# Performance work log

Hardware: AMD Instinct MI355X
Metric: run time of the kernel (lower is better)

Reference implementation:

```python
import jax, jax.numpy as jnp
import numpy as np

# Qwen3-VL-MoE text experts (training path): token permute -> grouped GEMM
# (gate_up) -> SwiGLU -> grouped GEMM (down) -> token unpermute + prob combine.
# Routing is generated perfectly balanced (each expert receives exactly M/E
# expanded tokens) so the grouped GEMM over the sorted token buffer is exactly
# a batched matmul over E contiguous groups -- same math as npu_grouped_matmul.

E, H, D, T, K = 32, 2048, 768, 4096, 8  # experts, hidden, moe_intermediate, tokens, top_k
M = T * K                                # expanded rows


def setup_inputs() -> dict:
    key = jax.random.key(0)
    k1, k2, k3, k4, k5 = jax.random.split(key, 5)
    hidden_states = jax.random.normal(k1, (T, H), dtype=jnp.float32)
    routing_weights = jax.nn.softmax(jax.random.normal(k2, (T, E), dtype=jnp.float32), axis=-1)
    # balanced expert assignment: each expert id appears exactly M // E times
    flat = jnp.tile(jnp.arange(E, dtype=jnp.int32), M // E)
    router_indices = jax.random.permutation(k3, flat).reshape(T, K)
    gate_up_proj = jax.random.normal(k4, (E, H, 2 * D), dtype=jnp.float32) * 0.02
    down_proj = jax.random.normal(k5, (E, D, H), dtype=jnp.float32) * 0.02
    return {
        "hidden_states": hidden_states,
        "routing_weights": routing_weights,
        "router_indices": router_indices,
        "gate_up_proj": gate_up_proj,
        "down_proj": down_proj,
    }


def reference(hidden_states, routing_weights, router_indices, gate_up_proj, down_proj):
    n_tok, hid = hidden_states.shape
    n_exp = gate_up_proj.shape[0]
    top_k = router_indices.shape[1]
    n_rows = n_tok * top_k
    grp = n_rows // n_exp  # balanced group size

    # --- npu_moe_token_permute: sort expanded (token, slot) rows by expert id
    flat_experts = router_indices.reshape(-1)            # (M,)
    order = jnp.argsort(flat_experts)                    # stable sort by expert
    permuted = hidden_states[order // top_k]             # (M, H)

    # --- grouped GEMM #1 (gate_up): balanced groups -> batched matmul
    xg = permuted.reshape(n_exp, grp, hid)               # (E, g, H)
    gate_up = jnp.einsum('egh,ehd->egd', xg, gate_up_proj)  # (E, g, 2D)

    # --- npu_swiglu(dim=-1): silu(first half) * second half
    gate, up = jnp.split(gate_up, 2, axis=-1)
    act = jax.nn.silu(gate) * up                         # (E, g, D)

    # --- grouped GEMM #2 (down)
    out = jnp.einsum('egd,edh->egh', act, down_proj).reshape(n_rows, hid)

    # --- npu_moe_token_unpermute: invert permutation, combine with probs
    inv = jnp.argsort(order)
    expanded = out[inv].reshape(n_tok, top_k, hid)       # (T, K, H)
    probs = jnp.take_along_axis(routing_weights, router_indices, axis=1)  # (T, K)
    return jnp.einsum('tkh,tk->th', expanded, probs)     # (T, H)
```

## Files before the change

### kernel.cpp

```cpp
#include <hip/hip_runtime.h>
#include <hip/hip_bf16.h>
#include <cstdint>


#define E_   32
#define H_   2048
#define D_   768
#define T_   4096
#define K_   8
#define M_   (T_ * K_)
#define G_   (M_ / E_)
#define GU2  (2 * D_)

typedef unsigned short u16;
typedef short bf16x8 __attribute__((ext_vector_type(8)));
typedef float f32x4 __attribute__((ext_vector_type(4)));
typedef unsigned short u16x2 __attribute__((ext_vector_type(2)));
typedef unsigned short u16x8 __attribute__((ext_vector_type(8)));

__device__ __forceinline__ u16 f2bf(float f) {
  unsigned u = __float_as_uint(f);
  u += 0x7FFFu + ((u >> 16) & 1u);
  return (u16)(u >> 16);
}
__device__ __forceinline__ float bf2f(u16 v) {
  return __uint_as_float(((unsigned)v) << 16);
}

#define GLOAD16(g, l) __builtin_amdgcn_global_load_lds(                        \
    (const __attribute__((address_space(1))) void*)(g),                        \
    (__attribute__((address_space(3))) void*)(l), 16, 0, 0)

#define VM8()   asm volatile("s_waitcnt vmcnt(8)" ::: "memory")
#define VM4()   asm volatile("s_waitcnt vmcnt(4)" ::: "memory")
#define VM0()   asm volatile("s_waitcnt vmcnt(0)" ::: "memory")
#define LGKM0() asm volatile("s_waitcnt lgkmcnt(0)" ::: "memory")
#define SCHB()  __builtin_amdgcn_sched_barrier(0)
#define BAR()   __builtin_amdgcn_s_barrier()

__global__ __launch_bounds__(256) void cvt_hidden(const float* __restrict__ in,
                                                  u16* __restrict__ out) {
  const int i = blockIdx.x * 256 + threadIdx.x;
  const float4 v = ((const float4*)in)[i];
  u16x2 a; a.x = f2bf(v.x); a.y = f2bf(v.y);
  u16x2 b; b.x = f2bf(v.z); b.y = f2bf(v.w);
  *(u16x2*)&out[(size_t)i * 4]     = a;
  *(u16x2*)&out[(size_t)i * 4 + 2] = b;
}

__global__ __launch_bounds__(256) void transpose_cvt(const float* __restrict__ in,
                                                     u16* __restrict__ out,
                                                     int R, int C, int mode) {
  __shared__ u16 tl[64 * 72];
  const int b = blockIdx.z;
  const int c0 = blockIdx.x * 64, r0 = blockIdx.y * 64;
  const int tid = threadIdx.x;
  const float* ip = in + ((size_t)b * R + r0) * C + c0;
  const int rr4 = tid >> 4;
  const int cc4 = (tid & 15) * 4;
#pragma unroll
  for (int p = 0; p < 4; ++p) {
    const int r = p * 16 + rr4;
    const float4 v = *(const float4*)&ip[(size_t)r * C + cc4];
    tl[(cc4 + 0) * 72 + r] = f2bf(v.x);
    tl[(cc4 + 1) * 72 + r] = f2bf(v.y);
    tl[(cc4 + 2) * 72 + r] = f2bf(v.z);
    tl[(cc4 + 3) * 72 + r] = f2bf(v.w);
  }
  __syncthreads();
  const int rs = (tid & 7) * 8;
#pragma unroll
  for (int q = 0; q < 2; ++q) {
    const int c = q * 32 + (tid >> 3);
    const int gc = c0 + c;
    int rr;
    if (mode == 1) {
      const int j = (gc < D_) ? gc : (gc - D_);
      rr = (j >> 4) * 32 + ((gc < D_) ? 0 : 16) + (j & 15);
    } else {
      rr = gc;
    }
    const u16x8 v = *(const u16x8*)&tl[c * 72 + rs];
    *(u16x8*)&out[((size_t)b * C + rr) * R + r0 + rs] = v;
  }
}

__global__ __launch_bounds__(256) void build_perm(const int* __restrict__ ridx,
                                                  int* __restrict__ perm_src) {
  const int e = blockIdx.x;
  const int lane = threadIdx.x & 63, wid = threadIdx.x >> 6;
  __shared__ int wcnt[4];
  __shared__ int running;
  if (threadIdx.x == 0) running = 0;
  __syncthreads();
  for (int base = 0; base < M_; base += 256) {
    const int i = base + threadIdx.x;
    const bool match = (ridx[i] == e);
    const unsigned long long mask = __ballot(match);
    if (lane == 0) wcnt[wid] = __popcll(mask);
    __syncthreads();
    int wpre = 0;
    for (int w0 = 0; w0 < wid; ++w0) wpre += wcnt[w0];
    const int rank = __popcll(mask & ((1ull << lane) - 1ull));
    if (match) perm_src[e * G_ + running + wpre + rank] = i;
    __syncthreads();
    if (threadIdx.x == 0) running += wcnt[0] + wcnt[1] + wcnt[2] + wcnt[3];
    __syncthreads();
  }
}

__global__ __launch_bounds__(256) void gather_probs(const int* __restrict__ ridx,
                                                    const float* __restrict__ rw,
                                                    float* __restrict__ probs) {
  const int i = blockIdx.x * 256 + threadIdx.x;
  const int t = i >> 3;
  probs[i] = rw[t * E_ + ridx[i]];
}

__global__ __launch_bounds__(512, 2) void gemm1_swiglu(
    const u16* __restrict__ hid, const u16* __restrict__ gup,
    const int* __restrict__ perm, u16* __restrict__ act) {
  __shared__ u16 As[4][8192];
  __shared__ u16 Bs[4][8192];
  const int NT = H_ / 32;

  const int nwg = 6 * 4 * E_;
  const int wid = (blockIdx.x % 8) * (nwg / 8) + blockIdx.x / 8;
  const int e = wid / 24;
  const int mb = (wid / 6) % 4;
  const int nb = wid % 6;

  const int tid = threadIdx.x;
  const int lane = tid & 63, w = tid >> 6;
  const int wr = w >> 2, wc = w & 3;

  const int srow = tid >> 2, schunk = tid & 3;
  const u16* pA[2]; const u16* pB[2];
#pragma unroll
  for (int q = 0; q < 2; ++q) {
    const int r = q * 128 + srow;
    const int cg = (schunk ^ ((r >> 1) & 3)) * 8;
    const int token = perm[e * G_ + mb * 256 + r] >> 3;
    pA[q] = hid + (size_t)token * H_ + cg;
    pB[q] = gup + ((size_t)e * GU2 + nb * 256 + r) * H_ + cg;
  }

  int aoff[8], boff[4];
  {
    const int l15 = lane & 15, hk = lane >> 4;
#pragma unroll
    for (int m = 0; m < 8; ++m) {
      const int rA = wr * 128 + m * 16 + l15;
      aoff[m] = rA * 32 + ((hk ^ ((rA >> 1) & 3)) * 8);
    }
#pragma unroll
    for (int n = 0; n < 4; ++n) {
      const int rB = wc * 64 + n * 16 + l15;
      boff[n] = rB * 32 + ((hk ^ ((rB >> 1) & 3)) * 8);
    }
  }

  f32x4 acc[8][4];
#pragma unroll
  for (int m = 0; m < 8; ++m)
#pragma unroll
    for (int n = 0; n < 4; ++n) acc[m][n] = (f32x4){0.f, 0.f, 0.f, 0.f};

  GLOAD16(pA[0], &As[0][tid * 8]);      GLOAD16(pA[1], &As[0][4096 + tid * 8]);
  GLOAD16(pB[0], &Bs[0][tid * 8]);      GLOAD16(pB[1], &Bs[0][4096 + tid * 8]);
  GLOAD16(pA[0] + 32, &As[1][tid * 8]); GLOAD16(pA[1] + 32, &As[1][4096 + tid * 8]);
  GLOAD16(pB[0] + 32, &Bs[1][tid * 8]); GLOAD16(pB[1] + 32, &Bs[1][4096 + tid * 8]);
  GLOAD16(pA[0] + 64, &As[2][tid * 8]); GLOAD16(pA[1] + 64, &As[2][4096 + tid * 8]);
  GLOAD16(pB[0] + 64, &Bs[2][tid * 8]); GLOAD16(pB[1] + 64, &Bs[2][4096 + tid * 8]);
  VM8(); BAR(); SCHB();

#pragma unroll 4
  for (int t = 0; t < NT; ++t) {
    const int slot = t & 3, ts = (t + 3) & 3;
    const bool st = (t + 3) < NT;
    const u16* Ab = As[slot]; const u16* Bb = Bs[slot];
    bf16x8 av[4], bv[4];
#pragma unroll
    for (int n = 0; n < 4; ++n) bv[n] = *(const bf16x8*)&Bb[boff[n]];
#pragma unroll
    for (int m = 0; m < 4; ++m) av[m] = *(const bf16x8*)&Ab[aoff[m]];
    if (st) {
      GLOAD16(pA[0] + (t + 3) * 32, &As[ts][tid * 8]);
      GLOAD16(pA[1] + (t + 3) * 32, &As[ts][4096 + tid * 8]);
    }
    SCHB(); BAR(); LGKM0(); SCHB();
    __builtin_amdgcn_s_setprio(1);
#pragma unroll
    for (int m = 0; m < 4; ++m)
#pragma unroll
      for (int n = 0; n < 4; ++n)
        acc[m][n] = __builtin_amdgcn_mfma_f32_16x16x32_bf16(av[m], bv[n],
                                                            acc[m][n], 0, 0, 0);
    __builtin_amdgcn_s_setprio(0);
    SCHB(); BAR();
#pragma unroll
    for (int m = 0; m < 4; ++m) av[m] = *(const bf16x8*)&Ab[aoff[m + 4]];
    if (st) {
      GLOAD16(pB[0] + (t + 3) * 32, &Bs[ts][tid * 8]);
      GLOAD16(pB[1] + (t + 3) * 32, &Bs[ts][4096 + tid * 8]);
    }
    SCHB(); BAR(); LGKM0(); SCHB();
    __builtin_amdgcn_s_setprio(1);
#pragma unroll
    for (int m = 0; m < 4; ++m)
#pragma unroll
      for (int n = 0; n < 4; ++n)
        acc[m + 4][n] = __builtin_amdgcn_mfma_f32_16x16x32_bf16(av[m], bv[n],
                                                                acc[m + 4][n], 0, 0, 0);
    __builtin_amdgcn_s_setprio(0);
    SCHB();
    if (t + 3 < NT)      { VM8(); }
    else if (t + 2 < NT) { VM4(); }
    else                 { VM0(); }
    BAR();
  }

  const int lrow = (lane >> 4) * 4, lcol = lane & 15;
#pragma unroll
  for (int m = 0; m < 8; ++m)
#pragma unroll
    for (int p = 0; p < 2; ++p)
#pragma unroll
      for (int r = 0; r < 4; ++r) {
        const float g = acc[m][2 * p][r];
        const float u = acc[m][2 * p + 1][r];
        const float a_ = g / (1.f + __expf(-g)) * u;
        const int row = mb * 256 + wr * 128 + m * 16 + lrow + r;
        const int dcol = (nb * 8 + wc * 2 + p) * 16 + lcol;
        act[((size_t)e * G_ + row) * D_ + dcol] = f2bf(a_);
      }
}

__global__ __launch_bounds__(512, 2) void gemm2_scatter(
    const u16* __restrict__ act, const u16* __restrict__ dwn,
    const int* __restrict__ perm, u16* __restrict__ expo) {
  __shared__ u16 As[4][8192];
  __shared__ u16 Bs[4][8192];
  const int NT = D_ / 32;

  const int nwg = 8 * 4 * E_;
  const int wid = (blockIdx.x % 8) * (nwg / 8) + blockIdx.x / 8;
  const int e = wid / 32;
  const int mb = (wid / 8) % 4;
  const int nb = wid % 8;

  const int tid = threadIdx.x;
  const int lane = tid & 63, w = tid >> 6;
  const int wr = w >> 2, wc = w & 3;

  const int srow = tid >> 2, schunk = tid & 3;
  const u16* pA[2]; const u16* pB[2];
#pragma unroll
  for (int q = 0; q < 2; ++q) {
    const int r = q * 128 + srow;
    const int cg = (schunk ^ ((r >> 1) & 3)) * 8;
    pA[q] = act + ((size_t)e * G_ + mb * 256 + r) * D_ + cg;
    pB[q] = dwn + ((size_t)e * H_ + nb * 256 + r) * D_ + cg;
  }

  int aoff[8], boff[4];
  {
    const int l15 = lane & 15, hk = lane >> 4;
#pragma unroll
    for (int m = 0; m < 8; ++m) {
      const int rA = wr * 128 + m * 16 + l15;
      aoff[m] = rA * 32 + ((hk ^ ((rA >> 1) & 3)) * 8);
    }
#pragma unroll
    for (int n = 0; n < 4; ++n) {
      const int rB = wc * 64 + n * 16 + l15;
      boff[n] = rB * 32 + ((hk ^ ((rB >> 1) & 3)) * 8);
    }
  }

  f32x4 acc[8][4];
#pragma unroll
  for (int m = 0; m < 8; ++m)
#pragma unroll
    for (int n = 0; n < 4; ++n) acc[m][n] = (f32x4){0.f, 0.f, 0.f, 0.f};

  GLOAD16(pA[0], &As[0][tid * 8]);      GLOAD16(pA[1], &As[0][4096 + tid * 8]);
  GLOAD16(pB[0], &Bs[0][tid * 8]);      GLOAD16(pB[1], &Bs[0][4096 + tid * 8]);
  GLOAD16(pA[0] + 32, &As[1][tid * 8]); GLOAD16(pA[1] + 32, &As[1][4096 + tid * 8]);
  GLOAD16(pB[0] + 32, &Bs[1][tid * 8]); GLOAD16(pB[1] + 32, &Bs[1][4096 + tid * 8]);
  GLOAD16(pA[0] + 64, &As[2][tid * 8]); GLOAD16(pA[1] + 64, &As[2][4096 + tid * 8]);
  GLOAD16(pB[0] + 64, &Bs[2][tid * 8]); GLOAD16(pB[1] + 64, &Bs[2][4096 + tid * 8]);
  VM8(); BAR(); SCHB();

#pragma unroll 4
  for (int t = 0; t < NT; ++t) {
    const int slot = t & 3, ts = (t + 3) & 3;
    const bool st = (t + 3) < NT;
    const u16* Ab = As[slot]; const u16* Bb = Bs[slot];
    bf16x8 av[4], bv[4];
#pragma unroll
    for (int n = 0; n < 4; ++n) bv[n] = *(const bf16x8*)&Bb[boff[n]];
#pragma unroll
    for (int m = 0; m < 4; ++m) av[m] = *(const bf16x8*)&Ab[aoff[m]];
    if (st) {
      GLOAD16(pA[0] + (t + 3) * 32, &As[ts][tid * 8]);
      GLOAD16(pA[1] + (t + 3) * 32, &As[ts][4096 + tid * 8]);
    }
    SCHB(); BAR(); LGKM0(); SCHB();
    __builtin_amdgcn_s_setprio(1);
#pragma unroll
    for (int m = 0; m < 4; ++m)
#pragma unroll
      for (int n = 0; n < 4; ++n)
        acc[m][n] = __builtin_amdgcn_mfma_f32_16x16x32_bf16(av[m], bv[n],
                                                            acc[m][n], 0, 0, 0);
    __builtin_amdgcn_s_setprio(0);
    SCHB(); BAR();
#pragma unroll
    for (int m = 0; m < 4; ++m) av[m] = *(const bf16x8*)&Ab[aoff[m + 4]];
    if (st) {
      GLOAD16(pB[0] + (t + 3) * 32, &Bs[ts][tid * 8]);
      GLOAD16(pB[1] + (t + 3) * 32, &Bs[ts][4096 + tid * 8]);
    }
    SCHB(); BAR(); LGKM0(); SCHB();
    __builtin_amdgcn_s_setprio(1);
#pragma unroll
    for (int m = 0; m < 4; ++m)
#pragma unroll
      for (int n = 0; n < 4; ++n)
        acc[m + 4][n] = __builtin_amdgcn_mfma_f32_16x16x32_bf16(av[m], bv[n],
                                                                acc[m + 4][n], 0, 0, 0);
    __builtin_amdgcn_s_setprio(0);
    SCHB();
    if (t + 3 < NT)      { VM8(); }
    else if (t + 2 < NT) { VM4(); }
    else                 { VM0(); }
    BAR();
  }

  const int lrow = (lane >> 4) * 4, lcol = lane & 15;
#pragma unroll
  for (int m = 0; m < 8; ++m)
#pragma unroll
    for (int r = 0; r < 4; ++r) {
      const int dst = e * G_ + mb * 256 + wr * 128 + m * 16 + lrow + r;
      const int src = perm[dst];
      u16* orow = expo + (size_t)src * H_ + nb * 256 + wc * 64;
#pragma unroll
      for (int n = 0; n < 4; ++n)
        orow[n * 16 + lcol] = f2bf(acc[m][n][r]);
    }
}

__global__ __launch_bounds__(256) void combine(const u16* __restrict__ expo,
                                               const float* __restrict__ probs,
                                               float* __restrict__ out) {
  const int t = blockIdx.x;
  const int h0 = threadIdx.x * 8;
  float r[8] = {0.f, 0.f, 0.f, 0.f, 0.f, 0.f, 0.f, 0.f};
#pragma unroll
  for (int k = 0; k < K_; ++k) {
    const float p = probs[t * K_ + k];
    const u16x8 v = *(const u16x8*)&expo[((size_t)(t * K_ + k)) * H_ + h0];
#pragma unroll
    for (int j = 0; j < 8; ++j) r[j] += p * bf2f(v[j]);
  }
  float4 o0 = {r[0], r[1], r[2], r[3]};
  float4 o1 = {r[4], r[5], r[6], r[7]};
  *(float4*)&out[(size_t)t * H_ + h0]     = o0;
  *(float4*)&out[(size_t)t * H_ + h0 + 4] = o1;
}

extern "C" void kernel_launch(void* const* d_in, const int* in_sizes, int n_in,
                              void* d_out, int out_size, void* d_ws, size_t ws_size,
                              hipStream_t stream) {
  const float* hidden = (const float*)d_in[0];
  const float* rw     = (const float*)d_in[1];
  const int*   ridx   = (const int*)d_in[2];
  const float* gup_f  = (const float*)d_in[3];
  const float* dwn_f  = (const float*)d_in[4];
  float* out = (float*)d_out;

  char* ws = (char*)d_ws;
  size_t off = 0;
  auto alloc = [&](size_t bytes) -> void* {
    void* p = ws + off;
    off += (bytes + 255) & ~(size_t)255;
    return p;
  };
  u16*   hid_bf = (u16*)alloc((size_t)T_ * H_ * 2);
  u16*   gup_t  = (u16*)alloc((size_t)E_ * GU2 * H_ * 2);
  u16*   dwn_t  = (u16*)alloc((size_t)E_ * H_ * D_ * 2);
  u16*   act    = (u16*)alloc((size_t)M_ * D_ * 2);
  u16*   expo   = (u16*)alloc((size_t)M_ * H_ * 2);
  int*   perm   = (int*)alloc((size_t)M_ * 4);
  float* probs  = (float*)alloc((size_t)M_ * 4);
  if (off > ws_size) return;

  cvt_hidden<<<(T_ * H_ / 4) / 256, 256, 0, stream>>>(hidden, hid_bf);
  transpose_cvt<<<dim3(GU2 / 64, H_ / 64, E_), 256, 0, stream>>>(gup_f, gup_t, H_, GU2, 1);
  transpose_cvt<<<dim3(H_ / 64, D_ / 64, E_), 256, 0, stream>>>(dwn_f, dwn_t, D_, H_, 0);
  build_perm<<<E_, 256, 0, stream>>>(ridx, perm);
  gather_probs<<<M_ / 256, 256, 0, stream>>>(ridx, rw, probs);
  gemm1_swiglu<<<6 * 4 * E_, 512, 0, stream>>>(hid_bf, gup_t, perm, act);
  gemm2_scatter<<<8 * 4 * E_, 512, 0, stream>>>(act, dwn_t, perm, expo);
  combine<<<T_, 256, 0, stream>>>(expo, probs, out);
}
```

Measured before the change: 618.6 us.

## Switch grouped GEMMs to 32x32 MFMA and parallelize permutation build

Result: faster. 564.2 us (-8.8%).

```diff
diff --git a/kernel.cpp b/kernel.cpp
--- a/kernel.cpp
+++ b/kernel.cpp
@@ -14,7 +14,7 @@
 
 typedef unsigned short u16;
 typedef short bf16x8 __attribute__((ext_vector_type(8)));
-typedef float f32x4 __attribute__((ext_vector_type(4)));
+typedef float f32x16 __attribute__((ext_vector_type(16)));
 typedef unsigned short u16x2 __attribute__((ext_vector_type(2)));
 typedef unsigned short u16x8 __attribute__((ext_vector_type(8)));
 
@@ -76,7 +76,7 @@
     int rr;
     if (mode == 1) {
       const int j = (gc < D_) ? gc : (gc - D_);
-      rr = (j >> 4) * 32 + ((gc < D_) ? 0 : 16) + (j & 15);
+      rr = (j >> 5) * 64 + ((gc < D_) ? 0 : 32) + (j & 31);
     } else {
       rr = gc;
     }
@@ -85,36 +85,21 @@
   }
 }
 
-__global__ __launch_bounds__(256) void build_perm(const int* __restrict__ ridx,
-                                                  int* __restrict__ perm_src) {
-  const int e = blockIdx.x;
-  const int lane = threadIdx.x & 63, wid = threadIdx.x >> 6;
-  __shared__ int wcnt[4];
-  __shared__ int running;
-  if (threadIdx.x == 0) running = 0;
+__global__ __launch_bounds__(256) void build_perm_fast(const int* __restrict__ ridx,
+                                                       int* __restrict__ perm,
+                                                       int* __restrict__ gcnt) {
+  __shared__ int lc[E_];
+  __shared__ int lb[E_];
+  const int tid = threadIdx.x;
+  if (tid < E_) lc[tid] = 0;
   __syncthreads();
-  for (int base = 0; base < M_; base += 256) {
-    const int i = base + threadIdx.x;
-    const bool match = (ridx[i] == e);
-    const unsigned long long mask = __ballot(match);
-    if (lane == 0) wcnt[wid] = __popcll(mask);
-    __syncthreads();
-    int wpre = 0;
-    for (int w0 = 0; w0 < wid; ++w0) wpre += wcnt[w0];
-    const int rank = __popcll(mask & ((1ull << lane) - 1ull));
-    if (match) perm_src[e * G_ + running + wpre + rank] = i;
-    __syncthreads();
-    if (threadIdx.x == 0) running += wcnt[0] + wcnt[1] + wcnt[2] + wcnt[3];
-    __syncthreads();
-  }
-}
-
-__global__ __launch_bounds__(256) void gather_probs(const int* __restrict__ ridx,
-                                                    const float* __restrict__ rw,
-                                                    float* __restrict__ probs) {
-  const int i = blockIdx.x * 256 + threadIdx.x;
-  const int t = i >> 3;
-  probs[i] = rw[t * E_ + ridx[i]];
+  const int i = blockIdx.x * 256 + tid;
+  const int e = ridx[i];
+  const int p = atomicAdd(&lc[e], 1);
+  __syncthreads();
+  if (tid < E_) lb[tid] = atomicAdd(&gcnt[tid], lc[tid]);
+  __syncthreads();
+  perm[e * G_ + lb[e] + p] = i;
 }
 
 __global__ __launch_bounds__(512, 2) void gemm1_swiglu(
@@ -145,26 +130,30 @@
     pB[q] = gup + ((size_t)e * GU2 + nb * 256 + r) * H_ + cg;
   }
 
-  int aoff[8], boff[4];
-  {
-    const int l15 = lane & 15, hk = lane >> 4;
-#pragma unroll
-    for (int m = 0; m < 8; ++m) {
-      const int rA = wr * 128 + m * 16 + l15;
-      aoff[m] = rA * 32 + ((hk ^ ((rA >> 1) & 3)) * 8);
-    }
-#pragma unroll
-    for (int n = 0; n < 4; ++n) {
-      const int rB = wc * 64 + n * 16 + l15;
-      boff[n] = rB * 32 + ((hk ^ ((rB >> 1) & 3)) * 8);
-    }
-  }
-
-  f32x4 acc[8][4];
-#pragma unroll
-  for (int m = 0; m < 8; ++m)
-#pragma unroll
-    for (int n = 0; n < 4; ++n) acc[m][n] = (f32x4){0.f, 0.f, 0.f, 0.f};
+  const int l31 = lane & 31, hi = lane >> 5;
+  int aoff[4][2], boff[2][2];
+#pragma unroll
+  for (int m = 0; m < 4; ++m) {
+    const int rA = wr * 128 + m * 32 + l31;
+#pragma unroll
+    for (int ks = 0; ks < 2; ++ks)
+      aoff[m][ks] = rA * 32 + (((ks * 2 + hi) ^ ((rA >> 1) & 3)) * 8);
+  }
+#pragma unroll
+  for (int n = 0; n < 2; ++n) {
+    const int rB = wc * 64 + n * 32 + l31;
+#pragma unroll
+    for (int ks = 0; ks < 2; ++ks)
+      boff[n][ks] = rB * 32 + (((ks * 2 + hi) ^ ((rB >> 1) & 3)) * 8);
+  }
+
+  f32x16 acc[4][2];
+#pragma unroll
+  for (int m = 0; m < 4; ++m)
+#pragma unroll
+    for (int n = 0; n < 2; ++n)
+#pragma unroll
+      for (int r = 0; r < 16; ++r) acc[m][n][r] = 0.f;
 
   GLOAD16(pA[0], &As[0][tid * 8]);      GLOAD16(pA[1], &As[0][4096 + tid * 8]);
   GLOAD16(pB[0], &Bs[0][tid * 8]);      GLOAD16(pB[1], &Bs[0][4096 + tid * 8]);
@@ -179,11 +168,11 @@
     const int slot = t & 3, ts = (t + 3) & 3;
     const bool st = (t + 3) < NT;
     const u16* Ab = As[slot]; const u16* Bb = Bs[slot];
-    bf16x8 av[4], bv[4];
-#pragma unroll
-    for (int n = 0; n < 4; ++n) bv[n] = *(const bf16x8*)&Bb[boff[n]];
-#pragma unroll
-    for (int m = 0; m < 4; ++m) av[m] = *(const bf16x8*)&Ab[aoff[m]];
+    bf16x8 av[4], bv[2];
+#pragma unroll
+    for (int n = 0; n < 2; ++n) bv[n] = *(const bf16x8*)&Bb[boff[n][0]];
+#pragma unroll
+    for (int m = 0; m < 4; ++m) av[m] = *(const bf16x8*)&Ab[aoff[m][0]];
     if (st) {
       GLOAD16(pA[0] + (t + 3) * 32, &As[ts][tid * 8]);
       GLOAD16(pA[1] + (t + 3) * 32, &As[ts][4096 + tid * 8]);
@@ -193,13 +182,15 @@
 #pragma unroll
     for (int m = 0; m < 4; ++m)
 #pragma unroll
-      for (int n = 0; n < 4; ++n)
-        acc[m][n] = __builtin_amdgcn_mfma_f32_16x16x32_bf16(av[m], bv[n],
+      for (int n = 0; n < 2; ++n)
+        acc[m][n] = __builtin_amdgcn_mfma_f32_32x32x16_bf16(av[m], bv[n],
                                                             acc[m][n], 0, 0, 0);
     __builtin_amdgcn_s_setprio(0);
     SCHB(); BAR();
 #pragma unroll
-    for (int m = 0; m < 4; ++m) av[m] = *(const bf16x8*)&Ab[aoff[m + 4]];
+    for (int n = 0; n < 2; ++n) bv[n] = *(const bf16x8*)&Bb[boff[n][1]];
+#pragma unroll
+    for (int m = 0; m < 4; ++m) av[m] = *(const bf16x8*)&Ab[aoff[m][1]];
     if (st) {
       GLOAD16(pB[0] + (t + 3) * 32, &Bs[ts][tid * 8]);
       GLOAD16(pB[1] + (t + 3) * 32, &Bs[ts][4096 + tid * 8]);
@@ -209,9 +200,9 @@
 #pragma unroll
     for (int m = 0; m < 4; ++m)
 #pragma unroll
-      for (int n = 0; n < 4; ++n)
-        acc[m + 4][n] = __builtin_amdgcn_mfma_f32_16x16x32_bf16(av[m], bv[n],
-                                                                acc[m + 4][n], 0, 0, 0);
+      for (int n = 0; n < 2; ++n)
+        acc[m][n] = __builtin_amdgcn_mfma_f32_32x32x16_bf16(av[m], bv[n],
+                                                            acc[m][n], 0, 0, 0);
     __builtin_amdgcn_s_setprio(0);
     SCHB();
     if (t + 3 < NT)      { VM8(); }
@@ -220,20 +211,17 @@
     BAR();
   }
 
-  const int lrow = (lane >> 4) * 4, lcol = lane & 15;
-#pragma unroll
-  for (int m = 0; m < 8; ++m)
-#pragma unroll
-    for (int p = 0; p < 2; ++p)
-#pragma unroll
-      for (int r = 0; r < 4; ++r) {
-        const float g = acc[m][2 * p][r];
-        const float u = acc[m][2 * p + 1][r];
-        const float a_ = g / (1.f + __expf(-g)) * u;
-        const int row = mb * 256 + wr * 128 + m * 16 + lrow + r;
-        const int dcol = (nb * 8 + wc * 2 + p) * 16 + lcol;
-        act[((size_t)e * G_ + row) * D_ + dcol] = f2bf(a_);
-      }
+#pragma unroll
+  for (int m = 0; m < 4; ++m)
+#pragma unroll
+    for (int r = 0; r < 16; ++r) {
+      const float g = acc[m][0][r];
+      const float u = acc[m][1][r];
+      const float a_ = g / (1.f + __expf(-g)) * u;
+      const int row = mb * 256 + wr * 128 + m * 32 + (r & 3) + 8 * (r >> 2) + 4 * hi;
+      const int dcol = (nb * 4 + wc) * 32 + l31;
+      act[((size_t)e * G_ + row) * D_ + dcol] = f2bf(a_);
+    }
 }
 
 __global__ __launch_bounds__(512, 2) void gemm2_scatter(
@@ -263,26 +251,30 @@
     pB[q] = dwn + ((size_t)e * H_ + nb * 256 + r) * D_ + cg;
   }
 
-  int aoff[8], boff[4];
-  {
-    const int l15 = lane & 15, hk = lane >> 4;
-#pragma unroll
-    for (int m = 0; m < 8; ++m) {
-      const int rA = wr * 128 + m * 16 + l15;
-      aoff[m] = rA * 32 + ((hk ^ ((rA >> 1) & 3)) * 8);
-    }
-#pragma unroll
-    for (int n = 0; n < 4; ++n) {
-      const int rB = wc * 64 + n * 16 + l15;
-      boff[n] = rB * 32 + ((hk ^ ((rB >> 1) & 3)) * 8);
-    }
-  }
-
-  f32x4 acc[8][4];
-#pragma unroll
-  for (int m = 0; m < 8; ++m)
-#pragma unroll
-    for (int n = 0; n < 4; ++n) acc[m][n] = (f32x4){0.f, 0.f, 0.f, 0.f};
+  const int l31 = lane & 31, hi = lane >> 5;
+  int aoff[4][2], boff[2][2];
+#pragma unroll
+  for (int m = 0; m < 4; ++m) {
+    const int rA = wr * 128 + m * 32 + l31;
+#pragma unroll
+    for (int ks = 0; ks < 2; ++ks)
+      aoff[m][ks] = rA * 32 + (((ks * 2 + hi) ^ ((rA >> 1) & 3)) * 8);
+  }
+#pragma unroll
+  for (int n = 0; n < 2; ++n) {
+    const int rB = wc * 64 + n * 32 + l31;
+#pragma unroll
+    for (int ks = 0; ks < 2; ++ks)
+      boff[n][ks] = rB * 32 + (((ks * 2 + hi) ^ ((rB >> 1) & 3)) * 8);
+  }
+
+  f32x16 acc[4][2];
+#pragma unroll
+  for (int m = 0; m < 4; ++m)
+#pragma unroll
+    for (int n = 0; n < 2; ++n)
+#pragma unroll
+      for (int r = 0; r < 16; ++r) acc[m][n][r] = 0.f;
 
   GLOAD16(pA[0], &As[0][tid * 8]);      GLOAD16(pA[1], &As[0][4096 + tid * 8]);
   GLOAD16(pB[0], &Bs[0][tid * 8]);      GLOAD16(pB[1], &Bs[0][4096 + tid * 8]);
@@ -297,11 +289,11 @@
     const int slot = t & 3, ts = (t + 3) & 3;
     const bool st = (t + 3) < NT;
     const u16* Ab = As[slot]; const u16* Bb = Bs[slot];
-    bf16x8 av[4], bv[4];
-#pragma unroll
-    for (int n = 0; n < 4; ++n) bv[n] = *(const bf16x8*)&Bb[boff[n]];
-#pragma unroll
-    for (int m = 0; m < 4; ++m) av[m] = *(const bf16x8*)&Ab[aoff[m]];
+    bf16x8 av[4], bv[2];
+#pragma unroll
+    for (int n = 0; n < 2; ++n) bv[n] = *(const bf16x8*)&Bb[boff[n][0]];
+#pragma unroll
+    for (int m = 0; m < 4; ++m) av[m] = *(const bf16x8*)&Ab[aoff[m][0]];
     if (st) {
       GLOAD16(pA[0] + (t + 3) * 32, &As[ts][tid * 8]);
       GLOAD16(pA[1] + (t + 3) * 32, &As[ts][4096 + tid * 8]);
@@ -311,13 +303,15 @@
 #pragma unroll
     for (int m = 0; m < 4; ++m)
 #pragma unroll
-      for (int n = 0; n < 4; ++n)
-        acc[m][n] = __builtin_amdgcn_mfma_f32_16x16x32_bf16(av[m], bv[n],
+      for (int n = 0; n < 2; ++n)
+        acc[m][n] = __builtin_amdgcn_mfma_f32_32x32x16_bf16(av[m], bv[n],
                                                             acc[m][n], 0, 0, 0);
     __builtin_amdgcn_s_setprio(0);
     SCHB(); BAR();
 #pragma unroll
-    for (int m = 0; m < 4; ++m) av[m] = *(const bf16x8*)&Ab[aoff[m + 4]];
+    for (int n = 0; n < 2; ++n) bv[n] = *(const bf16x8*)&Bb[boff[n][1]];
+#pragma unroll
+    for (int m = 0; m < 4; ++m) av[m] = *(const bf16x8*)&Ab[aoff[m][1]];
     if (st) {
       GLOAD16(pB[0] + (t + 3) * 32, &Bs[ts][tid * 8]);
       GLOAD16(pB[1] + (t + 3) * 32, &Bs[ts][4096 + tid * 8]);
@@ -327,9 +321,9 @@
 #pragma unroll
     for (int m = 0; m < 4; ++m)
 #pragma unroll
-      for (int n = 0; n < 4; ++n)
-        acc[m + 4][n] = __builtin_amdgcn_mfma_f32_16x16x32_bf16(av[m], bv[n],
-                                                                acc[m + 4][n], 0, 0, 0);
+      for (int n = 0; n < 2; ++n)
+        acc[m][n] = __builtin_amdgcn_mfma_f32_32x32x16_bf16(av[m], bv[n],
+                                                            acc[m][n], 0, 0, 0);
     __builtin_amdgcn_s_setprio(0);
     SCHB();
     if (t + 3 < NT)      { VM8(); }
@@ -338,29 +332,34 @@
     BAR();
   }
 
-  const int lrow = (lane >> 4) * 4, lcol = lane & 15;
-#pragma unroll
-  for (int m = 0; m < 8; ++m)
-#pragma unroll
-    for (int r = 0; r < 4; ++r) {
-      const int dst = e * G_ + mb * 256 + wr * 128 + m * 16 + lrow + r;
+#pragma unroll
+  for (int m = 0; m < 4; ++m)
+#pragma unroll
+    for (int r = 0; r < 16; ++r) {
+      const int row = wr * 128 + m * 32 + (r & 3) + 8 * (r >> 2) + 4 * hi;
+      const int dst = e * G_ + mb * 256 + row;
       const int src = perm[dst];
       u16* orow = expo + (size_t)src * H_ + nb * 256 + wc * 64;
 #pragma unroll
-      for (int n = 0; n < 4; ++n)
-        orow[n * 16 + lcol] = f2bf(acc[m][n][r]);
+      for (int n = 0; n < 2; ++n)
+        orow[n * 32 + l31] = f2bf(acc[m][n][r]);
     }
 }
 
 __global__ __launch_bounds__(256) void combine(const u16* __restrict__ expo,
-                                               const float* __restrict__ probs,
+                                               const int* __restrict__ ridx,
+                                               const float* __restrict__ rw,
                                                float* __restrict__ out) {
+  __shared__ float pr[K_];
   const int t = blockIdx.x;
+  if (threadIdx.x < K_)
+    pr[threadIdx.x] = rw[t * E_ + ridx[t * K_ + threadIdx.x]];
+  __syncthreads();
   const int h0 = threadIdx.x * 8;
   float r[8] = {0.f, 0.f, 0.f, 0.f, 0.f, 0.f, 0.f, 0.f};
 #pragma unroll
   for (int k = 0; k < K_; ++k) {
-    const float p = probs[t * K_ + k];
+    const float p = pr[k];
     const u16x8 v = *(const u16x8*)&expo[((size_t)(t * K_ + k)) * H_ + h0];
 #pragma unroll
     for (int j = 0; j < 8; ++j) r[j] += p * bf2f(v[j]);
@@ -394,15 +393,15 @@
   u16*   act    = (u16*)alloc((size_t)M_ * D_ * 2);
   u16*   expo   = (u16*)alloc((size_t)M_ * H_ * 2);
   int*   perm   = (int*)alloc((size_t)M_ * 4);
-  float* probs  = (float*)alloc((size_t)M_ * 4);
+  int*   gcnt   = (int*)alloc((size_t)E_ * 4);
   if (off > ws_size) return;
 
+  hipMemsetAsync(gcnt, 0, E_ * sizeof(int), stream);
   cvt_hidden<<<(T_ * H_ / 4) / 256, 256, 0, stream>>>(hidden, hid_bf);
   transpose_cvt<<<dim3(GU2 / 64, H_ / 64, E_), 256, 0, stream>>>(gup_f, gup_t, H_, GU2, 1);
   transpose_cvt<<<dim3(H_ / 64, D_ / 64, E_), 256, 0, stream>>>(dwn_f, dwn_t, D_, H_, 0);
-  build_perm<<<E_, 256, 0, stream>>>(ridx, perm);
-  gather_probs<<<M_ / 256, 256, 0, stream>>>(ridx, rw, probs);
+  build_perm_fast<<<M_ / 256, 256, 0, stream>>>(ridx, perm, gcnt);
   gemm1_swiglu<<<6 * 4 * E_, 512, 0, stream>>>(hid_bf, gup_t, perm, act);
   gemm2_scatter<<<8 * 4 * E_, 512, 0, stream>>>(act, dwn_t, perm, expo);
-  combine<<<T_, 256, 0, stream>>>(expo, probs, out);
-}
+  combine<<<T_, 256, 0, stream>>>(expo, ridx, rw, out);
+}
```
